# Performance work log

Measured on AMD Instinct MI355X. Metric: run time of the kernel, lower is better.

Reference implementation:

```python
import jax, jax.numpy as jnp
import numpy as np


def _fp_levels(ebits: int, mbits: int) -> np.ndarray:
    """All finite values of an IEEE-like float format (subnormals + normals, single zero)."""
    bias = (1 << (ebits - 1)) - 1
    maxE = (1 << ebits) - 1
    vals = {0.0}
    for sgn in (-1.0, 1.0):
        for F in range(1, 1 << mbits):  # subnormals
            vals.add(sgn * 2.0 ** (1 - bias) * (F / float(1 << mbits)))
        for E in range(1, maxE):  # normals (top exponent excluded: inf/nan)
            for F in range(0, 1 << mbits):
                vals.add(sgn * 2.0 ** (E - bias) * (1.0 + F / float(1 << mbits)))
    return np.array(sorted(vals), dtype=np.float32)


LEVELS_E4M3 = jnp.asarray(_fp_levels(4, 3))  # L = 239 sorted finite levels


def setup_inputs() -> dict:
    key = jax.random.key(0)
    x = jax.random.normal(key, (4096, 8192), dtype=jnp.float32)
    return {"x": x}


def reference(x):
    levels = LEVELS_E4M3.astype(x.dtype)
    L = levels.shape[0]
    max_level = jnp.max(jnp.abs(levels))

    # First forward call: calibrated=False -> ema_maxabs is copied from cur = max|x|.
    # EMA update is under torch.no_grad -> constant w.r.t. x.
    ema = jax.lax.stop_gradient(jnp.max(jnp.abs(x)))
    s = jnp.maximum(ema / (max_level + 1e-12), 1e-8)  # per-tensor scale

    x_scaled = x / s

    # Nearest-level lookup. Equivalent to abs-diff argmin over all L levels, but O(log L)
    # per element via searchsorted on the sorted level table. Ties (exact midpoints)
    # resolve to the LOWER index, matching torch argmin's first-occurrence rule.
    i = jnp.searchsorted(levels, x_scaled)
    lo = jnp.clip(i - 1, 0, L - 1)
    hi = jnp.clip(i, 0, L - 1)
    d_lo = jnp.abs(x_scaled - levels[lo])
    d_hi = jnp.abs(x_scaled - levels[hi])
    idx = jnp.where(d_lo <= d_hi, lo, hi)

    xq = levels[idx] * s
    # STE.forward(xq) == xq + (xq.detach() - xq).detach() == xq in value.
    return xq
```

## Files before the change

### kernel.cpp

```cpp
#include <hip/hip_runtime.h>


typedef float f32x4 __attribute__((ext_vector_type(4)));

#define FP8Q_THREADS 256
#define FP8Q_MAXBLOCKS 2048

__global__ __launch_bounds__(FP8Q_THREADS) void fp8q_absmax_kernel(
    const f32x4* __restrict__ x4, float* __restrict__ partials,
    const float* __restrict__ x_tail, int n4, int ntail)
{
    __shared__ float smem[FP8Q_THREADS / 64];
    int tid = blockIdx.x * blockDim.x + threadIdx.x;
    int stride = gridDim.x * blockDim.x;
    float m = 0.0f;
    for (int i = tid; i < n4; i += stride) {
        f32x4 v = x4[i];
        m = fmaxf(m, fmaxf(fmaxf(fabsf(v.x), fabsf(v.y)),
                           fmaxf(fabsf(v.z), fabsf(v.w))));
    }
    if (tid < ntail) m = fmaxf(m, fabsf(x_tail[tid]));
    #pragma unroll
    for (int off = 32; off > 0; off >>= 1)
        m = fmaxf(m, __shfl_xor(m, off));
    if ((threadIdx.x & 63) == 0) smem[threadIdx.x >> 6] = m;
    __syncthreads();
    if (threadIdx.x == 0) {
        float mm = smem[0];
        #pragma unroll
        for (int w = 1; w < FP8Q_THREADS / 64; ++w) mm = fmaxf(mm, smem[w]);
        partials[blockIdx.x] = mm;
    }
}

__device__ __forceinline__ float fp8q_quant1(float x, float s)
{
    float v = x / s;
    v = fminf(fmaxf(v, -240.0f), 240.0f);
    float m = fabsf(v);
    int e  = (int)(__float_as_uint(m) >> 23) - 127;
    int se = e - 3;
    if (se < -9) se = -9;
    float step     = __uint_as_float((unsigned int)(se + 127) << 23);
    float inv_step = __uint_as_float((unsigned int)(127 - se) << 23);
    float k = v * inv_step;
    float n = ceilf(k - 0.5f);
    return (n * step) * s;
}

__global__ __launch_bounds__(FP8Q_THREADS) void fp8q_quant_kernel(
    const f32x4* __restrict__ x4, f32x4* __restrict__ o4,
    const float* __restrict__ x_tail, float* __restrict__ o_tail,
    const float* __restrict__ partials, int np, int n4, int ntail)
{
    __shared__ float smem[FP8Q_THREADS / 64];
    __shared__ float s_shared;
    float m = 0.0f;
    for (int i = threadIdx.x; i < np; i += FP8Q_THREADS)
        m = fmaxf(m, partials[i]);
    #pragma unroll
    for (int off = 32; off > 0; off >>= 1)
        m = fmaxf(m, __shfl_xor(m, off));
    if ((threadIdx.x & 63) == 0) smem[threadIdx.x >> 6] = m;
    __syncthreads();
    if (threadIdx.x == 0) {
        float mm = smem[0];
        #pragma unroll
        for (int w = 1; w < FP8Q_THREADS / 64; ++w) mm = fmaxf(mm, smem[w]);
        s_shared = fmaxf(mm / 240.0f, 1e-8f);
    }
    __syncthreads();
    float s = s_shared;

    int tid = blockIdx.x * blockDim.x + threadIdx.x;
    int stride = gridDim.x * blockDim.x;
    for (int i = tid; i < n4; i += stride) {
        f32x4 v = x4[i];
        f32x4 r;
        r.x = fp8q_quant1(v.x, s);
        r.y = fp8q_quant1(v.y, s);
        r.z = fp8q_quant1(v.z, s);
        r.w = fp8q_quant1(v.w, s);
        __builtin_nontemporal_store(r, &o4[i]);
    }
    if (tid < ntail) o_tail[tid] = fp8q_quant1(x_tail[tid], s);
}

extern "C" void kernel_launch(void* const* d_in, const int* in_sizes, int n_in,
                              void* d_out, int out_size, void* d_ws, size_t ws_size,
                              hipStream_t stream)
{
    const float* x = (const float*)d_in[0];
    float* out = (float*)d_out;
    int n = in_sizes[0];
    int n4 = n >> 2;
    int ntail = n & 3;
    const float* x_tail = x + (size_t)n4 * 4;
    float* o_tail = out + (size_t)n4 * 4;

    float* partials = (float*)d_ws;

    int blocks = (n4 + FP8Q_THREADS - 1) / FP8Q_THREADS;
    if (blocks > FP8Q_MAXBLOCKS) blocks = FP8Q_MAXBLOCKS;
    if (blocks < 1) blocks = 1;

    fp8q_absmax_kernel<<<blocks, FP8Q_THREADS, 0, stream>>>(
        (const f32x4*)x, partials, x_tail, n4, ntail);
    fp8q_quant_kernel<<<blocks, FP8Q_THREADS, 0, stream>>>(
        (const f32x4*)x, (f32x4*)out, x_tail, o_tail, partials, blocks, n4, ntail);
}
```

Measured before the change: 68.92 us.

## Fuse absmax and quantize kernels with a cooperative grid sync

Merges the two-kernel pipeline (absmax partials, then quantize) into one cooperative kernel that writes per-block maxima, syncs the whole grid, and has every block reduce the partials itself. It removes one kernel launch and the inter-kernel gap, and caps the grid at the occupancy limit. The trade-offs are the cost of the grid-wide barrier, a smaller grid, host-side occupancy queries on every call, and the fact that each block now re-reads all partials.

```diff
diff --git a/kernel.cpp b/kernel.cpp
--- a/kernel.cpp
+++ b/kernel.cpp
@@ -1,4 +1,7 @@
 #include <hip/hip_runtime.h>
+#include <hip/hip_cooperative_groups.h>
+
+namespace cg = cooperative_groups;
 
 
 typedef float f32x4 __attribute__((ext_vector_type(4)));
@@ -6,13 +9,30 @@
 #define FP8Q_THREADS 256
 #define FP8Q_MAXBLOCKS 2048
 
-__global__ __launch_bounds__(FP8Q_THREADS) void fp8q_absmax_kernel(
-    const f32x4* __restrict__ x4, float* __restrict__ partials,
-    const float* __restrict__ x_tail, int n4, int ntail)
+__device__ __forceinline__ float fp8q_quant1(float x, float s)
+{
+    float v = x / s;
+    v = fminf(fmaxf(v, -240.0f), 240.0f);
+    float m = fabsf(v);
+    int e  = (int)(__float_as_uint(m) >> 23) - 127;
+    int se = e - 3;
+    if (se < -9) se = -9;
+    float step     = __uint_as_float((unsigned int)(se + 127) << 23);
+    float inv_step = __uint_as_float((unsigned int)(127 - se) << 23);
+    float k = v * inv_step;
+    float n = ceilf(k - 0.5f);
+    return (n * step) * s;
+}
+
+__global__ __launch_bounds__(FP8Q_THREADS) void fp8q_fused_kernel(
+    const f32x4* __restrict__ x4, f32x4* __restrict__ o4,
+    const float* __restrict__ x_tail, float* __restrict__ o_tail,
+    float* __restrict__ partials, int n4, int ntail)
 {
     __shared__ float smem[FP8Q_THREADS / 64];
     int tid = blockIdx.x * blockDim.x + threadIdx.x;
     int stride = gridDim.x * blockDim.x;
+
     float m = 0.0f;
     for (int i = tid; i < n4; i += stride) {
         f32x4 v = x4[i];
@@ -29,51 +49,26 @@
         float mm = smem[0];
         #pragma unroll
         for (int w = 1; w < FP8Q_THREADS / 64; ++w) mm = fmaxf(mm, smem[w]);
-        partials[blockIdx.x] = mm;
+        __hip_atomic_store(&partials[blockIdx.x], mm, __ATOMIC_RELAXED,
+                           __HIP_MEMORY_SCOPE_AGENT);
     }
-}
 
-__device__ __forceinline__ float fp8q_quant1(float x, float s)
-{
-    float v = x / s;
-    v = fminf(fmaxf(v, -240.0f), 240.0f);
-    float m = fabsf(v);
-    int e  = (int)(__float_as_uint(m) >> 23) - 127;
-    int se = e - 3;
-    if (se < -9) se = -9;
-    float step     = __uint_as_float((unsigned int)(se + 127) << 23);
-    float inv_step = __uint_as_float((unsigned int)(127 - se) << 23);
-    float k = v * inv_step;
-    float n = ceilf(k - 0.5f);
-    return (n * step) * s;
-}
+    cg::this_grid().sync();
 
-__global__ __launch_bounds__(FP8Q_THREADS) void fp8q_quant_kernel(
-    const f32x4* __restrict__ x4, f32x4* __restrict__ o4,
-    const float* __restrict__ x_tail, float* __restrict__ o_tail,
-    const float* __restrict__ partials, int np, int n4, int ntail)
-{
-    __shared__ float smem[FP8Q_THREADS / 64];
-    __shared__ float s_shared;
-    float m = 0.0f;
-    for (int i = threadIdx.x; i < np; i += FP8Q_THREADS)
-        m = fmaxf(m, partials[i]);
+    float mp = 0.0f;
+    for (int i = threadIdx.x; i < (int)gridDim.x; i += blockDim.x)
+        mp = fmaxf(mp, __hip_atomic_load(&partials[i], __ATOMIC_RELAXED,
+                                         __HIP_MEMORY_SCOPE_AGENT));
     #pragma unroll
     for (int off = 32; off > 0; off >>= 1)
-        m = fmaxf(m, __shfl_xor(m, off));
-    if ((threadIdx.x & 63) == 0) smem[threadIdx.x >> 6] = m;
+        mp = fmaxf(mp, __shfl_xor(mp, off));
+    if ((threadIdx.x & 63) == 0) smem[threadIdx.x >> 6] = mp;
     __syncthreads();
-    if (threadIdx.x == 0) {
-        float mm = smem[0];
-        #pragma unroll
-        for (int w = 1; w < FP8Q_THREADS / 64; ++w) mm = fmaxf(mm, smem[w]);
-        s_shared = fmaxf(mm / 240.0f, 1e-8f);
-    }
-    __syncthreads();
-    float s = s_shared;
+    float mm = smem[0];
+    #pragma unroll
+    for (int w = 1; w < FP8Q_THREADS / 64; ++w) mm = fmaxf(mm, smem[w]);
+    float s = fmaxf(mm / 240.0f, 1e-8f);
 
-    int tid = blockIdx.x * blockDim.x + threadIdx.x;
-    int stride = gridDim.x * blockDim.x;
     for (int i = tid; i < n4; i += stride) {
         f32x4 v = x4[i];
         f32x4 r;
@@ -97,15 +92,26 @@
     int ntail = n & 3;
     const float* x_tail = x + (size_t)n4 * 4;
     float* o_tail = out + (size_t)n4 * 4;
+    float* partials = (float*)d_ws;
 
-    float* partials = (float*)d_ws;
+    int dev = 0;
+    (void)hipGetDevice(&dev);
+    int num_cu = 256;
+    (void)hipDeviceGetAttribute(&num_cu, hipDeviceAttributeMultiprocessorCount, dev);
+    int max_per_cu = 4;
+    (void)hipOccupancyMaxActiveBlocksPerMultiprocessor(&max_per_cu, fp8q_fused_kernel,
+                                                       FP8Q_THREADS, 0);
+    if (max_per_cu < 1) max_per_cu = 1;
 
     int blocks = (n4 + FP8Q_THREADS - 1) / FP8Q_THREADS;
     if (blocks > FP8Q_MAXBLOCKS) blocks = FP8Q_MAXBLOCKS;
+    if (blocks > max_per_cu * num_cu) blocks = max_per_cu * num_cu;
     if (blocks < 1) blocks = 1;
 
-    fp8q_absmax_kernel<<<blocks, FP8Q_THREADS, 0, stream>>>(
-        (const f32x4*)x, partials, x_tail, n4, ntail);
-    fp8q_quant_kernel<<<blocks, FP8Q_THREADS, 0, stream>>>(
-        (const f32x4*)x, (f32x4*)out, x_tail, o_tail, partials, blocks, n4, ntail);
+    const f32x4* x4 = (const f32x4*)x;
+    f32x4* o4 = (f32x4*)out;
+    void* args[] = { (void*)&x4, (void*)&o4, (void*)&x_tail, (void*)&o_tail,
+                     (void*)&partials, (void*)&n4, (void*)&ntail };
+    (void)hipLaunchCooperativeKernel((void*)fp8q_fused_kernel, dim3(blocks),
+                                     dim3(FP8Q_THREADS), args, 0, stream);
 }
```

Measured after the change: 267.7 us. 3.88x slower.
